# Kernel optimization log

Measured on AMD Instinct MI355X. Metric: run time of the kernel, lower is better.

The kernel has to match this reference:

```python
import jax, jax.numpy as jnp
import numpy as np

N = 20000          # num nodes
E = 250000         # num edges
B = 128            # num graphs in batch
Fin = 512
Fqk = 512
Fv = 512
H = 8              # nheads


def setup_inputs() -> dict:
    key = jax.random.key(0)
    k1, k2, k3, k4 = jax.random.split(key, 4)
    x = jax.random.normal(k1, (N, Fin), dtype=jnp.float32)
    batch = jnp.sort(jax.random.randint(k2, (N,), 0, B)).astype(jnp.int32)
    ei = jax.random.randint(k3, (2, E), 0, N).astype(jnp.int32)
    # proj weight of Linear(Fin, 2*Fqk+Fv, bias=False); stored as (Fin, Ftot)
    W = (jax.random.normal(k4, (Fin, 2 * Fqk + Fv), dtype=jnp.float32)
         / np.sqrt(Fin).astype(np.float32))
    return {"x": x, "batch": batch, "ei": ei, "W": W}


def reference(x, batch, ei, W):
    src, dest = ei[0], ei[1]
    n = x.shape[0]
    Fh = Fqk // H            # head dim for q/k
    Fhv = Fv // H            # head dim for v
    scaling = float(Fh) ** (-0.5)

    qkv = x @ W                                    # (N, 2*Fqk+Fv)
    q, k, v = jnp.split(qkv, [Fqk, 2 * Fqk], axis=-1)
    q = (q * scaling).reshape(n, H, Fh)
    k = k.reshape(n, H, Fh)
    v = v.reshape(n, H, Fhv)

    # edge-wise gathers
    qs = q[src]                                    # (E, H, Fh)
    ks = k[dest]                                   # (E, H, Fh)
    vs = v[dest]                                   # (E, H, Fhv)

    # per-edge, per-head attention scores
    aw = jnp.einsum('ehf,ehf->eh', qs, ks)         # (E, H)

    # segment softmax over edges sharing the same src node (stable)
    m = jax.ops.segment_max(aw, src, num_segments=n)       # (N, H)
    e = jnp.exp(aw - m[src])                                # (E, H)
    denom = jax.ops.segment_sum(e, src, num_segments=n)     # (N, H)
    alpha = e / denom[src]                                   # (E, H)

    # scatter-weighted aggregation of values back to src nodes
    out = jax.ops.segment_sum(alpha[:, :, None] * vs, src, num_segments=n)  # (N, H, Fhv)
    return out.reshape(n, Fv)
```

## Files before the change

kernel.cpp:

```cpp
#include <hip/hip_runtime.h>
#include <cstdint>

typedef float f32x4 __attribute__((ext_vector_type(4)));
typedef __bf16 bf16x8 __attribute__((ext_vector_type(8)));

__device__ __forceinline__ unsigned short f2b(float f) {
  unsigned int u = __float_as_uint(f);
  u = (u + 0x7fffu + ((u >> 16) & 1u)) >> 16;
  return (unsigned short)u;
}

__device__ __forceinline__ void unpack8(uint4 u, float* f) {
  f[0] = __uint_as_float((u.x & 0xffffu) << 16);
  f[1] = __uint_as_float(u.x & 0xffff0000u);
  f[2] = __uint_as_float((u.y & 0xffffu) << 16);
  f[3] = __uint_as_float(u.y & 0xffff0000u);
  f[4] = __uint_as_float((u.z & 0xffffu) << 16);
  f[5] = __uint_as_float(u.z & 0xffff0000u);
  f[6] = __uint_as_float((u.w & 0xffffu) << 16);
  f[7] = __uint_as_float(u.w & 0xffff0000u);
}

__device__ __forceinline__ void async_copy16(const void* g, void* l) {
  __builtin_amdgcn_global_load_lds(
      (const __attribute__((address_space(1))) void*)g,
      (__attribute__((address_space(3))) void*)l, 16, 0, 0);
}

__global__ __launch_bounds__(256) void prep_kernel(
    const float* __restrict__ W, unsigned short* __restrict__ Wt, int NT) {
  __shared__ float tile[32][33];
  int b = blockIdx.x, t = threadIdx.x;
  int tilesPerRow = NT / 32;
  int n0 = (b % tilesPerRow) * 32, k0 = (b / tilesPerRow) * 32;
  int r = t >> 5, c = t & 31;
#pragma unroll
  for (int ph = 0; ph < 4; ++ph)
    tile[r + 8 * ph][c] = W[(size_t)(k0 + r + 8 * ph) * NT + n0 + c];
  __syncthreads();
#pragma unroll
  for (int ph = 0; ph < 4; ++ph) {
    int rr = r + 8 * ph;
    int nn = n0 + rr;
    float s = (nn < 512) ? 0.125f : 1.0f;
    Wt[(size_t)nn * 512 + k0 + c] = f2b(tile[c][rr] * s);
  }
}

__global__ __launch_bounds__(1024, 4) void gemm256_kernel(
    const float* __restrict__ X, const unsigned short* __restrict__ Bt,
    unsigned short* __restrict__ C, int K, int NT, int NPAN, int nrows,
    int GEMMB, const int* __restrict__ src, const int* __restrict__ dst,
    int* __restrict__ deg, int* __restrict__ edst, int E) {
  __shared__ __align__(16) unsigned short SM[49152];

  int bx = blockIdx.x, tid = threadIdx.x;

  if (bx >= GEMMB) {
    int e = (bx - GEMMB) * 1024 + tid;
    if (e < E) {
      int s = src[e], d = dst[e];
      int j = atomicAdd(&deg[s], 1);
      if (j < 64) edst[(size_t)s * 64 + j] = d;
    }
    return;
  }

  int nwg = GEMMB;
  int q8 = nwg >> 3, r8 = nwg & 7;
  int xcd = bx & 7, idx = bx >> 3;
  int wgid = (xcd < r8 ? xcd * (q8 + 1) : r8 * (q8 + 1) + (xcd - r8) * q8) + idx;
  int mtile = wgid / NPAN, npanel = wgid % NPAN;
  int m0 = mtile * 256, n0 = npanel * 256;

  int wave = tid >> 6, lane = tid & 63;
  int wm = wave >> 2, wn = wave & 3;
  int hi = lane >> 4, l15 = lane & 15;

  int srow = (tid >> 6) * 16 + l15;
  int scol = ((tid >> 4) & 3) * 8;
  bool inb = (m0 + srow) < nrows;
  const float* pX = X + (size_t)(m0 + srow) * K + scol;
  const unsigned short* pB = Bt + (size_t)(n0 + srow) * K + scol;

  auto loadA = [&](int t, float4& f0, float4& f1) {
    if (inb) {
      f0 = *(const float4*)(pX + t * 32);
      f1 = *(const float4*)(pX + t * 32 + 4);
    } else {
      f0 = make_float4(0.f, 0.f, 0.f, 0.f);
      f1 = make_float4(0.f, 0.f, 0.f, 0.f);
    }
  };
  auto cvtWriteA = [&](const float4& f0, const float4& f1, int slot) {
    uint4 w;
    w.x = (unsigned)f2b(f0.x) | ((unsigned)f2b(f0.y) << 16);
    w.y = (unsigned)f2b(f0.z) | ((unsigned)f2b(f0.w) << 16);
    w.z = (unsigned)f2b(f1.x) | ((unsigned)f2b(f1.y) << 16);
    w.w = (unsigned)f2b(f1.z) | ((unsigned)f2b(f1.w) << 16);
    *(uint4*)(SM + slot * 8192 + tid * 8) = w;
  };

  async_copy16(pB, SM + 24576 + tid * 8);
  async_copy16(pB + 32, SM + 24576 + 8192 + tid * 8);
  __builtin_amdgcn_sched_barrier(0);
  float4 f00, f01, nf0, nf1;
  loadA(0, f00, f01);
  loadA(1, nf0, nf1);
  __builtin_amdgcn_sched_barrier(0);
  cvtWriteA(f00, f01, 0);
  asm volatile("s_waitcnt lgkmcnt(0)" ::: "memory");
  __builtin_amdgcn_s_barrier();
  __builtin_amdgcn_sched_barrier(0);

  f32x4 acc[4][4] = {};
  int aoff = wm * 2048 + lane * 8;
  int boff = 24576 + wn * 2048 + lane * 8;

#pragma unroll
  for (int t = 0; t < 16; ++t) {
    int sb = (t % 3) * 8192;
    bf16x8 av[4], bv[4];
    const unsigned short* a_ = SM + sb + aoff;
    const unsigned short* b_ = SM + sb + boff;
#pragma unroll
    for (int i = 0; i < 4; ++i) av[i] = *(const bf16x8*)(a_ + i * 512);
#pragma unroll
    for (int j = 0; j < 4; ++j) bv[j] = *(const bf16x8*)(b_ + j * 512);
    if (t + 2 < 16) {
      int s2 = ((t + 2) % 3) * 8192;
      async_copy16(pB + (t + 2) * 32, SM + 24576 + s2 + tid * 8);
    }
    if (t + 1 < 16) cvtWriteA(nf0, nf1, (t + 1) % 3);
    if (t + 2 < 16) loadA(t + 2, nf0, nf1);
    __builtin_amdgcn_s_setprio(1);
#pragma unroll
    for (int i = 0; i < 4; ++i)
#pragma unroll
      for (int j = 0; j < 4; ++j)
        acc[i][j] = __builtin_amdgcn_mfma_f32_16x16x32_bf16(av[i], bv[j], acc[i][j], 0, 0, 0);
    __builtin_amdgcn_s_setprio(0);
    asm volatile("s_waitcnt lgkmcnt(0)" ::: "memory");
    __builtin_amdgcn_sched_barrier(0);
    __builtin_amdgcn_s_barrier();
    __builtin_amdgcn_sched_barrier(0);
  }

  __syncthreads();
  unsigned short* cs = SM + wave * 640;
  unsigned short* gC = C + (size_t)(m0 + wm * 64) * NT + n0 + wn * 64;
  int erow = lane >> 2, echunk = (lane & 3) * 8;
#pragma unroll
  for (int i = 0; i < 4; ++i)
#pragma unroll
    for (int p = 0; p < 2; ++p) {
#pragma unroll
      for (int jj = 0; jj < 2; ++jj)
#pragma unroll
        for (int q = 0; q < 4; ++q)
          cs[(hi * 4 + q) * 40 + jj * 16 + l15] = f2b(acc[i][2 * p + jj][q]);
      uint4 val = *(const uint4*)&cs[erow * 40 + echunk];
      *(uint4*)&gC[(size_t)(i * 16 + erow) * NT + p * 32 + echunk] = val;
    }
}

__global__ __launch_bounds__(256) void attn_kernel(
    const unsigned short* __restrict__ qkv, const int* __restrict__ deg,
    const int* __restrict__ edst, float* __restrict__ out, int n) {
  int wave = threadIdx.x >> 6, lane = threadIdx.x & 63;
  int node = blockIdx.x * 4 + wave;
  if (node >= n) return;

  float q[8];
  unpack8(*(const uint4*)(qkv + (size_t)node * 1536 + lane * 8), q);

  float acc[8] = {0.f, 0.f, 0.f, 0.f, 0.f, 0.f, 0.f, 0.f};
  float l = 0.f;
  int dn = deg[node];
  if (dn > 64) dn = 64;
  int beg = node * 64, end = beg + dn;

  int i = beg;
  for (; i + 4 <= end; i += 4) {
    int d0 = edst[i], d1 = edst[i + 1], d2 = edst[i + 2], d3 = edst[i + 3];
    const uint4* p0 = (const uint4*)(qkv + (size_t)d0 * 1536 + 512 + lane * 8);
    const uint4* p1 = (const uint4*)(qkv + (size_t)d1 * 1536 + 512 + lane * 8);
    const uint4* p2 = (const uint4*)(qkv + (size_t)d2 * 1536 + 512 + lane * 8);
    const uint4* p3 = (const uint4*)(qkv + (size_t)d3 * 1536 + 512 + lane * 8);
    uint4 kr0 = p0[0], vr0 = p0[64];
    uint4 kr1 = p1[0], vr1 = p1[64];
    uint4 kr2 = p2[0], vr2 = p2[64];
    uint4 kr3 = p3[0], vr3 = p3[64];
#pragma unroll
    for (int u = 0; u < 4; ++u) {
      uint4 kv = (u == 0) ? kr0 : (u == 1) ? kr1 : (u == 2) ? kr2 : kr3;
      uint4 vv = (u == 0) ? vr0 : (u == 1) ? vr1 : (u == 2) ? vr2 : vr3;
      float kf[8], vf[8];
      unpack8(kv, kf);
      unpack8(vv, vf);
      float part = 0.f;
#pragma unroll
      for (int j = 0; j < 8; ++j) part = fmaf(q[j], kf[j], part);
      part += __shfl_xor(part, 1);
      part += __shfl_xor(part, 2);
      part += __shfl_xor(part, 4);
      float p = __expf(part);
      l += p;
#pragma unroll
      for (int j = 0; j < 8; ++j) acc[j] = fmaf(p, vf[j], acc[j]);
    }
  }
  for (; i < end; ++i) {
    int d = edst[i];
    const uint4* pp = (const uint4*)(qkv + (size_t)d * 1536 + 512 + lane * 8);
    uint4 kv = pp[0], vv = pp[64];
    float kf[8], vf[8];
    unpack8(kv, kf);
    unpack8(vv, vf);
    float part = 0.f;
#pragma unroll
    for (int j = 0; j < 8; ++j) part = fmaf(q[j], kf[j], part);
    part += __shfl_xor(part, 1);
    part += __shfl_xor(part, 2);
    part += __shfl_xor(part, 4);
    float p = __expf(part);
    l += p;
#pragma unroll
    for (int j = 0; j < 8; ++j) acc[j] = fmaf(p, vf[j], acc[j]);
  }

  float inv = (l > 0.f) ? 1.f / l : 0.f;
  float4 o0, o1;
  o0.x = acc[0] * inv; o0.y = acc[1] * inv; o0.z = acc[2] * inv; o0.w = acc[3] * inv;
  o1.x = acc[4] * inv; o1.y = acc[5] * inv; o1.z = acc[6] * inv; o1.w = acc[7] * inv;
  float4* op = (float4*)(out + (size_t)node * 512 + lane * 8);
  op[0] = o0;
  op[1] = o1;
}

extern "C" void kernel_launch(void* const* d_in, const int* in_sizes, int n_in,
                              void* d_out, int out_size, void* d_ws, size_t ws_size,
                              hipStream_t stream) {
  const float* x = (const float*)d_in[0];
  const int* ei = (const int*)d_in[2];
  const float* W = (const float*)d_in[3];
  float* out = (float*)d_out;

  const int N = in_sizes[1];
  const int E = in_sizes[2] / 2;
  const int Fin = in_sizes[0] / N;
  const int FT = in_sizes[3] / Fin;
  const int MPAD = ((N + 255) / 256) * 256;

  const int* src = ei;
  const int* dst = ei + E;

  char* ws = (char*)d_ws;
  size_t off = 0;
  auto alloc = [&](size_t bytes) {
    void* p = ws + off;
    off = (off + bytes + 255) & ~(size_t)255;
    return p;
  };
  unsigned short* Wt  = (unsigned short*)alloc((size_t)FT * Fin * 2);
  unsigned short* qkv = (unsigned short*)alloc((size_t)MPAD * FT * 2);
  int* deg  = (int*)alloc((size_t)N * 4);
  int* edst = (int*)alloc((size_t)N * 64 * 4);

  hipMemsetAsync(deg, 0, (size_t)N * 4, stream);

  int nbConvw = (FT / 32) * (Fin / 32);
  prep_kernel<<<nbConvw, 256, 0, stream>>>(W, Wt, FT);

  int NPAN = FT / 256;
  int MTILES = MPAD / 256;
  int GEMMB = MTILES * NPAN;
  int nbBucket = (E + 1023) / 1024;
  gemm256_kernel<<<GEMMB + nbBucket, 1024, 0, stream>>>(
      x, Wt, qkv, Fin, FT, NPAN, N, GEMMB, src, dst, deg, edst, E);

  attn_kernel<<<(N + 3) / 4, 256, 0, stream>>>(qkv, deg, edst, out, N);
}
```

Baseline: 145.2 us.

## Make GEMM blocks process two M-tiles each and grid-stride edge bucketing

Each GEMM workgroup now loops over two 256-row M tiles that share the same N panel, halving the GEMM grid. The XCD-aware remap is simplified to assume GEMMB divisible by 8. The edge-bucketing blocks are cut to 16 and use a grid-stride loop. The attention kernel loads four edge indices with one int4 load. This aims to cut launch and tail overhead and spread the bucketing work, at the cost of less GEMM parallelism and a serial tail per block. The remap may mis-map blocks if GEMMB is not a multiple of 8.

```diff
diff --git a/kernel.cpp b/kernel.cpp
--- a/kernel.cpp
+++ b/kernel.cpp
@@ -50,15 +50,15 @@
 __global__ __launch_bounds__(1024, 4) void gemm256_kernel(
     const float* __restrict__ X, const unsigned short* __restrict__ Bt,
     unsigned short* __restrict__ C, int K, int NT, int NPAN, int nrows,
-    int GEMMB, const int* __restrict__ src, const int* __restrict__ dst,
+    int GEMMB, int NMG, int MTILES, int NBUCK,
+    const int* __restrict__ src, const int* __restrict__ dst,
     int* __restrict__ deg, int* __restrict__ edst, int E) {
   __shared__ __align__(16) unsigned short SM[49152];
 
   int bx = blockIdx.x, tid = threadIdx.x;
 
   if (bx >= GEMMB) {
-    int e = (bx - GEMMB) * 1024 + tid;
-    if (e < E) {
+    for (int e = (bx - GEMMB) * 1024 + tid; e < E; e += NBUCK * 1024) {
       int s = src[e], d = dst[e];
       int j = atomicAdd(&deg[s], 1);
       if (j < 64) edst[(size_t)s * 64 + j] = d;
@@ -66,12 +66,10 @@
     return;
   }
 
-  int nwg = GEMMB;
-  int q8 = nwg >> 3, r8 = nwg & 7;
-  int xcd = bx & 7, idx = bx >> 3;
-  int wgid = (xcd < r8 ? xcd * (q8 + 1) : r8 * (q8 + 1) + (xcd - r8) * q8) + idx;
-  int mtile = wgid / NPAN, npanel = wgid % NPAN;
-  int m0 = mtile * 256, n0 = npanel * 256;
+  int cpx = GEMMB >> 3;
+  int wgid = (bx & 7) * cpx + (bx >> 3);
+  int mg = wgid / NPAN, npanel = wgid % NPAN;
+  int n0 = npanel * 256;
 
   int wave = tid >> 6, lane = tid & 63;
   int wm = wave >> 2, wn = wave & 3;
@@ -79,89 +77,100 @@
 
   int srow = (tid >> 6) * 16 + l15;
   int scol = ((tid >> 4) & 3) * 8;
-  bool inb = (m0 + srow) < nrows;
-  const float* pX = X + (size_t)(m0 + srow) * K + scol;
   const unsigned short* pB = Bt + (size_t)(n0 + srow) * K + scol;
 
-  auto loadA = [&](int t, float4& f0, float4& f1) {
-    if (inb) {
-      f0 = *(const float4*)(pX + t * 32);
-      f1 = *(const float4*)(pX + t * 32 + 4);
-    } else {
-      f0 = make_float4(0.f, 0.f, 0.f, 0.f);
-      f1 = make_float4(0.f, 0.f, 0.f, 0.f);
-    }
-  };
-  auto cvtWriteA = [&](const float4& f0, const float4& f1, int slot) {
-    uint4 w;
-    w.x = (unsigned)f2b(f0.x) | ((unsigned)f2b(f0.y) << 16);
-    w.y = (unsigned)f2b(f0.z) | ((unsigned)f2b(f0.w) << 16);
-    w.z = (unsigned)f2b(f1.x) | ((unsigned)f2b(f1.y) << 16);
-    w.w = (unsigned)f2b(f1.z) | ((unsigned)f2b(f1.w) << 16);
-    *(uint4*)(SM + slot * 8192 + tid * 8) = w;
-  };
-
-  async_copy16(pB, SM + 24576 + tid * 8);
-  async_copy16(pB + 32, SM + 24576 + 8192 + tid * 8);
-  __builtin_amdgcn_sched_barrier(0);
-  float4 f00, f01, nf0, nf1;
-  loadA(0, f00, f01);
-  loadA(1, nf0, nf1);
-  __builtin_amdgcn_sched_barrier(0);
-  cvtWriteA(f00, f01, 0);
-  asm volatile("s_waitcnt lgkmcnt(0)" ::: "memory");
-  __builtin_amdgcn_s_barrier();
-  __builtin_amdgcn_sched_barrier(0);
-
-  f32x4 acc[4][4] = {};
   int aoff = wm * 2048 + lane * 8;
   int boff = 24576 + wn * 2048 + lane * 8;
-
-#pragma unroll
-  for (int t = 0; t < 16; ++t) {
-    int sb = (t % 3) * 8192;
-    bf16x8 av[4], bv[4];
-    const unsigned short* a_ = SM + sb + aoff;
-    const unsigned short* b_ = SM + sb + boff;
-#pragma unroll
-    for (int i = 0; i < 4; ++i) av[i] = *(const bf16x8*)(a_ + i * 512);
-#pragma unroll
-    for (int j = 0; j < 4; ++j) bv[j] = *(const bf16x8*)(b_ + j * 512);
-    if (t + 2 < 16) {
-      int s2 = ((t + 2) % 3) * 8192;
-      async_copy16(pB + (t + 2) * 32, SM + 24576 + s2 + tid * 8);
-    }
-    if (t + 1 < 16) cvtWriteA(nf0, nf1, (t + 1) % 3);
-    if (t + 2 < 16) loadA(t + 2, nf0, nf1);
-    __builtin_amdgcn_s_setprio(1);
-#pragma unroll
-    for (int i = 0; i < 4; ++i)
-#pragma unroll
-      for (int j = 0; j < 4; ++j)
-        acc[i][j] = __builtin_amdgcn_mfma_f32_16x16x32_bf16(av[i], bv[j], acc[i][j], 0, 0, 0);
-    __builtin_amdgcn_s_setprio(0);
+  int erow = lane >> 2, echunk = (lane & 3) * 8;
+
+#pragma unroll 1
+  for (int h = 0; h < 2; ++h) {
+    int mtile = mg + h * NMG;
+    if (mtile >= MTILES) break;
+    int m0 = mtile * 256;
+
+    bool inb = (m0 + srow) < nrows;
+    const float* pX = X + (size_t)(m0 + srow) * K + scol;
+
+    auto loadA = [&](int t, float4& f0, float4& f1) {
+      if (inb) {
+        f0 = *(const float4*)(pX + t * 32);
+        f1 = *(const float4*)(pX + t * 32 + 4);
+      } else {
+        f0 = make_float4(0.f, 0.f, 0.f, 0.f);
+        f1 = make_float4(0.f, 0.f, 0.f, 0.f);
+      }
+    };
+    auto cvtWriteA = [&](const float4& f0, const float4& f1, int slot) {
+      uint4 w;
+      w.x = (unsigned)f2b(f0.x) | ((unsigned)f2b(f0.y) << 16);
+      w.y = (unsigned)f2b(f0.z) | ((unsigned)f2b(f0.w) << 16);
+      w.z = (unsigned)f2b(f1.x) | ((unsigned)f2b(f1.y) << 16);
+      w.w = (unsigned)f2b(f1.z) | ((unsigned)f2b(f1.w) << 16);
+      *(uint4*)(SM + slot * 8192 + tid * 8) = w;
+    };
+
+    __syncthreads();
+
+    async_copy16(pB, SM + 24576 + tid * 8);
+    async_copy16(pB + 32, SM + 24576 + 8192 + tid * 8);
+    __builtin_amdgcn_sched_barrier(0);
+    float4 f00, f01, nf0, nf1;
+    loadA(0, f00, f01);
+    loadA(1, nf0, nf1);
+    __builtin_amdgcn_sched_barrier(0);
+    cvtWriteA(f00, f01, 0);
     asm volatile("s_waitcnt lgkmcnt(0)" ::: "memory");
-    __builtin_amdgcn_sched_barrier(0);
     __builtin_amdgcn_s_barrier();
     __builtin_amdgcn_sched_barrier(0);
-  }
-
-  __syncthreads();
-  unsigned short* cs = SM + wave * 640;
-  unsigned short* gC = C + (size_t)(m0 + wm * 64) * NT + n0 + wn * 64;
-  int erow = lane >> 2, echunk = (lane & 3) * 8;
-#pragma unroll
-  for (int i = 0; i < 4; ++i)
-#pragma unroll
-    for (int p = 0; p < 2; ++p) {
-#pragma unroll
-      for (int jj = 0; jj < 2; ++jj)
-#pragma unroll
-        for (int q = 0; q < 4; ++q)
-          cs[(hi * 4 + q) * 40 + jj * 16 + l15] = f2b(acc[i][2 * p + jj][q]);
-      uint4 val = *(const uint4*)&cs[erow * 40 + echunk];
-      *(uint4*)&gC[(size_t)(i * 16 + erow) * NT + p * 32 + echunk] = val;
+
+    f32x4 acc[4][4] = {};
+
+#pragma unroll
+    for (int t = 0; t < 16; ++t) {
+      int sb = (t % 3) * 8192;
+      bf16x8 av[4], bv[4];
+      const unsigned short* a_ = SM + sb + aoff;
+      const unsigned short* b_ = SM + sb + boff;
+#pragma unroll
+      for (int i = 0; i < 4; ++i) av[i] = *(const bf16x8*)(a_ + i * 512);
+#pragma unroll
+      for (int j = 0; j < 4; ++j) bv[j] = *(const bf16x8*)(b_ + j * 512);
+      if (t + 2 < 16) {
+        int s2 = ((t + 2) % 3) * 8192;
+        async_copy16(pB + (t + 2) * 32, SM + 24576 + s2 + tid * 8);
+      }
+      if (t + 1 < 16) cvtWriteA(nf0, nf1, (t + 1) % 3);
+      if (t + 2 < 16) loadA(t + 2, nf0, nf1);
+      __builtin_amdgcn_s_setprio(1);
+#pragma unroll
+      for (int i = 0; i < 4; ++i)
+#pragma unroll
+        for (int j = 0; j < 4; ++j)
+          acc[i][j] = __builtin_amdgcn_mfma_f32_16x16x32_bf16(av[i], bv[j], acc[i][j], 0, 0, 0);
+      __builtin_amdgcn_s_setprio(0);
+      asm volatile("s_waitcnt lgkmcnt(0)" ::: "memory");
+      __builtin_amdgcn_sched_barrier(0);
+      __builtin_amdgcn_s_barrier();
+      __builtin_amdgcn_sched_barrier(0);
     }
+
+    __syncthreads();
+    unsigned short* cs = SM + wave * 640;
+    unsigned short* gC = C + (size_t)(m0 + wm * 64) * NT + n0 + wn * 64;
+#pragma unroll
+    for (int i = 0; i < 4; ++i)
+#pragma unroll
+      for (int p = 0; p < 2; ++p) {
+#pragma unroll
+        for (int jj = 0; jj < 2; ++jj)
+#pragma unroll
+          for (int q = 0; q < 4; ++q)
+            cs[(hi * 4 + q) * 40 + jj * 16 + l15] = f2b(acc[i][2 * p + jj][q]);
+        uint4 val = *(const uint4*)&cs[erow * 40 + echunk];
+        *(uint4*)&gC[(size_t)(i * 16 + erow) * NT + p * 32 + echunk] = val;
+      }
+  }
 }
 
 __global__ __launch_bounds__(256) void attn_kernel(
@@ -182,11 +191,11 @@
 
   int i = beg;
   for (; i + 4 <= end; i += 4) {
-    int d0 = edst[i], d1 = edst[i + 1], d2 = edst[i + 2], d3 = edst[i + 3];
-    const uint4* p0 = (const uint4*)(qkv + (size_t)d0 * 1536 + 512 + lane * 8);
-    const uint4* p1 = (const uint4*)(qkv + (size_t)d1 * 1536 + 512 + lane * 8);
-    const uint4* p2 = (const uint4*)(qkv + (size_t)d2 * 1536 + 512 + lane * 8);
-    const uint4* p3 = (const uint4*)(qkv + (size_t)d3 * 1536 + 512 + lane * 8);
+    int4 dd = *(const int4*)&edst[i];
+    const uint4* p0 = (const uint4*)(qkv + (size_t)dd.x * 1536 + 512 + lane * 8);
+    const uint4* p1 = (const uint4*)(qkv + (size_t)dd.y * 1536 + 512 + lane * 8);
+    const uint4* p2 = (const uint4*)(qkv + (size_t)dd.z * 1536 + 512 + lane * 8);
+    const uint4* p3 = (const uint4*)(qkv + (size_t)dd.w * 1536 + 512 + lane * 8);
     uint4 kr0 = p0[0], vr0 = p0[64];
     uint4 kr1 = p1[0], vr1 = p1[64];
     uint4 kr2 = p2[0], vr2 = p2[64];
@@ -274,10 +283,12 @@
 
   int NPAN = FT / 256;
   int MTILES = MPAD / 256;
-  int GEMMB = MTILES * NPAN;
-  int nbBucket = (E + 1023) / 1024;
-  gemm256_kernel<<<GEMMB + nbBucket, 1024, 0, stream>>>(
-      x, Wt, qkv, Fin, FT, NPAN, N, GEMMB, src, dst, deg, edst, E);
+  int NMG = (MTILES + 1) / 2;
+  int GEMMB = NMG * NPAN;
+  int NBUCK = 16;
+  gemm256_kernel<<<GEMMB + NBUCK, 1024, 0, stream>>>(
+      x, Wt, qkv, Fin, FT, NPAN, N, GEMMB, NMG, MTILES, NBUCK,
+      src, dst, deg, edst, E);
 
   attn_kernel<<<(N + 3) / 4, 256, 0, stream>>>(qkv, deg, edst, out, N);
 }
```

After: 162.0 us. +11.6%, slower.
